# Performance work log

Hardware: AMD Instinct MI355X
Metric: run time of the kernel (lower is better)

The kernel has to match this reference:

```python
import jax, jax.numpy as jnp
import numpy as np

DIM = 1024
E = 8
HID = 4 * DIM  # DomainExpert FFN hidden size


def setup_inputs() -> dict:
    key = jax.random.key(0)
    ks = jax.random.split(key, 7)
    x = jax.random.normal(ks[0], (1, 2048, DIM), dtype=jnp.float32)
    Wr = jax.random.normal(ks[1], (DIM, E), dtype=jnp.float32) * (DIM ** -0.5)
    br = jnp.zeros((E,), dtype=jnp.float32)
    W1 = jax.random.normal(ks[2], (E, DIM, HID), dtype=jnp.float32) * (DIM ** -0.5)
    b1 = jnp.zeros((E, 1, HID), dtype=jnp.float32)
    W2 = jax.random.normal(ks[3], (E, HID, DIM), dtype=jnp.float32) * (HID ** -0.5)
    b2 = jnp.zeros((E, 1, DIM), dtype=jnp.float32)
    return {"x": x, "Wr": Wr, "br": br, "W1": W1, "b1": b1, "W2": W2, "b2": b2}


def reference(x, Wr, br, W1, b1, W2, b2):
    B, T, D = x.shape
    flat = x.reshape(B * T, D)                       # [N, D]
    logits = flat @ Wr + br                          # [N, E]
    z_loss = jnp.mean(jax.nn.logsumexp(logits, axis=-1) ** 2)
    probs = jax.nn.softmax(logits, axis=-1)          # eval path (no Gumbel)
    top_p, top_i = jax.lax.top_k(probs, 2)           # [N, 2]
    top_p = top_p / (top_p.sum(-1, keepdims=True) + 1e-12)
    N = flat.shape[0]
    nE = Wr.shape[1]
    # combine weights: w[t, e] = renormalized top-2 prob if e selected, else 0
    w = jnp.zeros((N, nE), dtype=flat.dtype).at[
        jnp.arange(N)[:, None], top_i].add(top_p)   # [N, E]
    # dense (jit-friendly) expert compute; combine masks out unselected experts
    h = jax.nn.gelu(jnp.einsum('td,edh->teh', flat, W1) + b1.transpose(1, 0, 2))  # [N, E, HID]
    y = jnp.einsum('teh,ehd->ted', h, W2) + b2.transpose(1, 0, 2)                 # [N, E, D]
    out = jnp.einsum('ted,te->td', y, w).reshape(B, T, D)
    importance = probs.mean(axis=0)                                               # [E]
    fi = jax.nn.one_hot(top_i, nE, dtype=flat.dtype).sum(axis=1).mean(axis=0)     # [E]
    aux_loss = jnp.asarray(nE, flat.dtype) * (importance * fi).sum()
    return out, z_loss, aux_loss
```

## Files before the change

kernel.cpp:

```cpp
#include <hip/hip_runtime.h>
#include <math.h>

#define N_TOK 2048
#define DIM   1024
#define NEXP  8
#define HID   4096
#define TOTPAIR (2 * N_TOK)

#define BM 128
#define BN 128
#define BK 32
#define KSPLIT2 4

typedef __bf16 bf16x8 __attribute__((ext_vector_type(8)));
typedef __bf16 bf16x4 __attribute__((ext_vector_type(4)));
typedef float  f32x4  __attribute__((ext_vector_type(4)));

__device__ __forceinline__ float gelu_tanh(float v) {
    float a = 0.7978845608028654f * (v + 0.044715f * v * v * v);
    a = fminf(fmaxf(a, -15.f), 15.f);
    float t = __expf(-2.f * a);
    return 0.5f * v * (1.f + (1.f - t) / (1.f + t));
}

__device__ __forceinline__ void stage16(const __bf16* g, __bf16* lds_base, int lane) {
#if defined(__has_builtin) && __has_builtin(__builtin_amdgcn_global_load_lds)
    __builtin_amdgcn_global_load_lds((const __attribute__((address_space(1))) void*)g,
                                     (__attribute__((address_space(3))) void*)lds_base,
                                     16, 0, 0);
#else
    *(bf16x8*)((char*)lds_base + (size_t)lane * 16) = *(const bf16x8*)g;
#endif
}

__device__ __forceinline__ int expert_prefix(const int* cnt, int e) {
    int s = 0;
    for (int i = 0; i < NEXP; i++) s += (i < e) ? cnt[i] : 0;
    return s;
}

__device__ __forceinline__ void router_body(
    int t, int lane,
    const float* __restrict__ x, const float* __restrict__ Wr, const float* __restrict__ br,
    float* __restrict__ probs, float* __restrict__ lsq,
    int* __restrict__ cnt, int* __restrict__ tok, float* __restrict__ wl) {
    const float* xr = x + (size_t)t * DIM;
    float acc[NEXP];
#pragma unroll
    for (int e = 0; e < NEXP; e++) acc[e] = 0.f;
    for (int d = lane; d < DIM; d += 64) {
        float xv = xr[d];
        const float* wr = Wr + (size_t)d * NEXP;
#pragma unroll
        for (int e = 0; e < NEXP; e++) acc[e] = fmaf(xv, wr[e], acc[e]);
    }
#pragma unroll
    for (int off = 32; off >= 1; off >>= 1) {
#pragma unroll
        for (int e = 0; e < NEXP; e++) acc[e] += __shfl_xor(acc[e], off, 64);
    }
    if (lane == 0) {
        float lg[NEXP], mx = -1e30f;
#pragma unroll
        for (int e = 0; e < NEXP; e++) { lg[e] = acc[e] + br[e]; mx = fmaxf(mx, lg[e]); }
        float se = 0.f, p[NEXP];
#pragma unroll
        for (int e = 0; e < NEXP; e++) { p[e] = expf(lg[e] - mx); se += p[e]; }
        float inv = 1.f / se;
        float lse = mx + logf(se);
        lsq[t] = lse * lse;
#pragma unroll
        for (int e = 0; e < NEXP; e++) probs[t * NEXP + e] = p[e] * inv;
        int i0 = 0;
#pragma unroll
        for (int e = 1; e < NEXP; e++) if (p[e] > p[i0]) i0 = e;
        int i1 = (i0 == 0) ? 1 : 0;
#pragma unroll
        for (int e = 0; e < NEXP; e++) if (e != i0 && p[e] > p[i1]) i1 = e;
        float p0 = p[i0] * inv, p1 = p[i1] * inv;
        float rn = 1.f / (p0 + p1 + 1e-12f);
        int pos0 = atomicAdd(&cnt[i0], 1);
        tok[i0 * N_TOK + pos0] = t;
        wl[i0 * N_TOK + pos0] = p0 * rn;
        int pos1 = atomicAdd(&cnt[i1], 1);
        tok[i1 * N_TOK + pos1] = t;
        wl[i1 * N_TOK + pos1] = p1 * rn;
    }
}

__global__ void router_kernel(const float* __restrict__ x, const float* __restrict__ Wr,
                              const float* __restrict__ br,
                              float* __restrict__ probs, float* __restrict__ lsq,
                              int* __restrict__ cnt, int* __restrict__ tok,
                              float* __restrict__ wl) {
    router_body(blockIdx.x, threadIdx.x, x, Wr, br, probs, lsq, cnt, tok, wl);
}

__global__ __launch_bounds__(256) void prep_kernel(
    const float* __restrict__ x, const float* __restrict__ Wr, const float* __restrict__ br,
    float* __restrict__ probs, float* __restrict__ lsq,
    int* __restrict__ cnt, int* __restrict__ tok, float* __restrict__ wl,
    __bf16* __restrict__ xb) {
    const int b = blockIdx.x;
    const int tid = threadIdx.x;
    if (b < 512) {
        int t = b * 4 + (tid >> 6);
        router_body(t, tid & 63, x, Wr, br, probs, lsq, cnt, tok, wl);
        return;
    }
    int idx = (b - 512) * 256 + tid;
    float4 v = ((const float4*)x)[idx];
    bf16x4 o;
    o.x = (__bf16)v.x; o.y = (__bf16)v.y; o.z = (__bf16)v.z; o.w = (__bf16)v.w;
    ((bf16x4*)xb)[idx] = o;
}

__global__ __launch_bounds__(256, 4) void gemm1_kernel(
    const __bf16* __restrict__ xb, const float* __restrict__ W1,
    const float* __restrict__ b1,
    const int* __restrict__ cnt,
    const int* __restrict__ tok, __bf16* __restrict__ h) {
    const int e = blockIdx.z;
    const int ce = cnt[e];
    const int mstart = blockIdx.y * BM;
    if (mstart >= ce) return;
    const int n0 = blockIdx.x * BN;
    const int offe = expert_prefix(cnt, e);

    __shared__ __bf16 smem[BM * 128];
    __shared__ int toksh[BM];
    __bf16* As = smem;
    __bf16* Bs = smem + 4096;

    const int tid = threadIdx.x;
    if (tid < BM) {
        int idx = mstart + tid;
        toksh[tid] = (idx < ce) ? tok[e * N_TOK + idx] : 0;
    }
    __syncthreads();

    const int lane = tid & 63;
    const int wid  = tid >> 6;
    const int row0 = (wid >> 1) * 64;
    const int col0 = (wid & 1) * 64;
    const int quad = lane >> 4;
    const int lcol = lane & 15;

    const int sub = lane >> 2;
    const int gk  = (((lane & 3) ^ (sub & 3)) << 3);
    const int ra0 = wid * 32 + sub;
    const int ra1 = ra0 + 16;
    const __bf16* pA0 = xb + (size_t)toksh[ra0] * DIM + gk;
    const __bf16* pA1 = xb + (size_t)toksh[ra1] * DIM + gk;
    __bf16* lA0 = &As[(wid * 2 + 0) * 512];
    __bf16* lA1 = &As[(wid * 2 + 1) * 512];

    const int khalf = (wid >> 1) * 16;
    const int nl    = (wid & 1) * 64 + lane;
    const float* __restrict__ W1e = W1 + (size_t)e * DIM * HID;
    const float* wsrc = W1e + (size_t)khalf * HID + n0 + nl;

    const int aswz = (quad ^ (lcol & 3)) << 3;
    const __bf16* aF = &As[(row0 + lcol) * BK + aswz];

    f32x4 acc[4][4];
#pragma unroll
    for (int i = 0; i < 4; i++)
#pragma unroll
        for (int j = 0; j < 4; j++) acc[i][j] = (f32x4){0.f, 0.f, 0.f, 0.f};

    for (int k0 = 0; k0 < DIM; k0 += BK) {
        float v[16];
        const float* ws = wsrc + (size_t)k0 * HID;
#pragma unroll
        for (int j = 0; j < 16; j++) v[j] = ws[(size_t)j * HID];
        stage16(pA0 + k0, lA0, lane);
        stage16(pA1 + k0, lA1, lane);
#pragma unroll
        for (int q = 0; q < 4; q++) {
            bf16x4 pk;
            pk.x = (__bf16)v[q * 4 + 0]; pk.y = (__bf16)v[q * 4 + 1];
            pk.z = (__bf16)v[q * 4 + 2]; pk.w = (__bf16)v[q * 4 + 3];
            int c = (wid >> 1) * 2 + (q >> 1);
            int slot = c ^ (nl & 3);
            *(bf16x4*)&Bs[slot * 1024 + nl * 8 + (q & 1) * 4] = pk;
        }
        __syncthreads();
        bf16x8 af[4], bfr[4];
#pragma unroll
        for (int i = 0; i < 4; i++) af[i]  = *(const bf16x8*)(aF + i * 16 * BK);
#pragma unroll
        for (int j = 0; j < 4; j++)
            bfr[j] = *(const bf16x8*)&Bs[((quad ^ (lcol & 3)) * 1024) + (col0 + j * 16 + lcol) * 8];
#pragma unroll
        for (int i = 0; i < 4; i++)
#pragma unroll
            for (int j = 0; j < 4; j++)
                acc[i][j] = __builtin_amdgcn_mfma_f32_16x16x32_bf16(af[i], bfr[j], acc[i][j], 0, 0, 0);
        __syncthreads();
    }

    const float* __restrict__ b1e = b1 + (size_t)e * HID;
    float bj[4];
#pragma unroll
    for (int j = 0; j < 4; j++) bj[j] = b1e[n0 + col0 + j * 16 + lcol];
#pragma unroll
    for (int i = 0; i < 4; i++)
#pragma unroll
        for (int reg = 0; reg < 4; reg++) {
            int row = row0 + i * 16 + quad * 4 + reg;
#pragma unroll
            for (int j = 0; j < 4; j++) {
                int col = col0 + j * 16 + lcol;
                int slot = (col >> 3) ^ (row & 15);
                smem[row * 128 + slot * 8 + (col & 7)] =
                    (__bf16)gelu_tanh(acc[i][j][reg] + bj[j]);
            }
        }
    __syncthreads();
    {
        int row = tid >> 1, half = tid & 1;
        int pos = mstart + row;
        if (pos < ce) {
            __bf16* hp = h + (size_t)(offe + pos) * HID + n0 + half * 64;
#pragma unroll
            for (int j = 0; j < 8; j++) {
                int chunk = half * 8 + j;
                int slot = chunk ^ (row & 15);
                *(bf16x8*)(hp + j * 8) = *(const bf16x8*)&smem[row * 128 + slot * 8];
            }
        }
    }
}

__global__ __launch_bounds__(256, 4) void gemm2_kernel(
    const __bf16* __restrict__ h, const float* __restrict__ W2,
    const float* __restrict__ b2,
    const int* __restrict__ cnt,
    const int* __restrict__ tok, const float* __restrict__ wl,
    float* __restrict__ out) {
    const int e = blockIdx.z >> 2;
    const int split = blockIdx.z & 3;
    const int ce = cnt[e];
    const int mstart = blockIdx.y * BM;
    if (mstart >= ce) return;
    const int n0 = blockIdx.x * BN;
    const int ks = split * (HID / KSPLIT2);
    const int offe = expert_prefix(cnt, e);

    __shared__ __bf16 As[BM * BK];
    __shared__ __bf16 Bs[4 * 128 * 8];
    __shared__ int   toksh[BM];
    __shared__ float wsh[BM];

    const int tid = threadIdx.x;
    if (tid < BM) {
        int idx = mstart + tid;
        toksh[tid] = (idx < ce) ? tok[e * N_TOK + idx] : 0;
        wsh[tid]   = (idx < ce) ? wl[e * N_TOK + idx] : 0.f;
    }
    __syncthreads();

    const int lane = tid & 63;
    const int wid  = tid >> 6;
    const int row0 = (wid >> 1) * 64;
    const int col0 = (wid & 1) * 64;
    const int quad = lane >> 4;
    const int lcol = lane & 15;

    const int sub = lane >> 2;
    const int gk  = (((lane & 3) ^ (sub & 3)) << 3);
    const int ra0 = wid * 32 + sub;
    const int ra1 = ra0 + 16;
    int hr0 = offe + mstart + ra0; if (hr0 >= TOTPAIR) hr0 = TOTPAIR - 1;
    int hr1 = offe + mstart + ra1; if (hr1 >= TOTPAIR) hr1 = TOTPAIR - 1;
    const __bf16* pA0 = h + (size_t)hr0 * HID + ks + gk;
    const __bf16* pA1 = h + (size_t)hr1 * HID + ks + gk;
    __bf16* lA0 = &As[(wid * 2 + 0) * 512];
    __bf16* lA1 = &As[(wid * 2 + 1) * 512];

    const int khalf = (wid >> 1) * 16;
    const int nl    = (wid & 1) * 64 + lane;
    const float* __restrict__ W2e = W2 + (size_t)e * HID * DIM;
    const float* wsrc = W2e + (size_t)(ks + khalf) * DIM + n0 + nl;

    const int aswz = (quad ^ (lcol & 3)) << 3;
    const __bf16* aF = &As[(row0 + lcol) * BK + aswz];

    f32x4 acc[4][4];
#pragma unroll
    for (int i = 0; i < 4; i++)
#pragma unroll
        for (int j = 0; j < 4; j++) acc[i][j] = (f32x4){0.f, 0.f, 0.f, 0.f};

    for (int k0 = 0; k0 < HID / KSPLIT2; k0 += BK) {
        float v[16];
        const float* ws = wsrc + (size_t)k0 * DIM;
#pragma unroll
        for (int j = 0; j < 16; j++) v[j] = ws[(size_t)j * DIM];
        stage16(pA0 + k0, lA0, lane);
        stage16(pA1 + k0, lA1, lane);
#pragma unroll
        for (int q = 0; q < 4; q++) {
            bf16x4 pk;
            pk.x = (__bf16)v[q * 4 + 0]; pk.y = (__bf16)v[q * 4 + 1];
            pk.z = (__bf16)v[q * 4 + 2]; pk.w = (__bf16)v[q * 4 + 3];
            int c = (wid >> 1) * 2 + (q >> 1);
            int slot = c ^ (nl & 3);
            *(bf16x4*)&Bs[slot * 1024 + nl * 8 + (q & 1) * 4] = pk;
        }
        __syncthreads();
        bf16x8 af[4], bfr[4];
#pragma unroll
        for (int i = 0; i < 4; i++) af[i]  = *(const bf16x8*)(aF + i * 16 * BK);
#pragma unroll
        for (int j = 0; j < 4; j++)
            bfr[j] = *(const bf16x8*)&Bs[((quad ^ (lcol & 3)) * 1024) + (col0 + j * 16 + lcol) * 8];
#pragma unroll
        for (int i = 0; i < 4; i++)
#pragma unroll
            for (int j = 0; j < 4; j++)
                acc[i][j] = __builtin_amdgcn_mfma_f32_16x16x32_bf16(af[i], bfr[j], acc[i][j], 0, 0, 0);
        __syncthreads();
    }

    const float* __restrict__ b2e = b2 + (size_t)e * DIM;
    const bool addBias = (split == 0);
#pragma unroll
    for (int i = 0; i < 4; i++) {
#pragma unroll
        for (int reg = 0; reg < 4; reg++) {
            int lrow = row0 + i * 16 + quad * 4 + reg;
            int pos = mstart + lrow;
            if (pos >= ce) continue;
            int tokm = toksh[lrow];
            float w = wsh[lrow];
#pragma unroll
            for (int j = 0; j < 4; j++) {
                int gcol = n0 + col0 + j * 16 + lcol;
                float vv = acc[i][j][reg] + (addBias ? b2e[gcol] : 0.f);
                atomicAdd(&out[(size_t)tokm * DIM + gcol], w * vv);
            }
        }
    }
}

__global__ __launch_bounds__(256, 2) void ffn_fallback_kernel(
    const float* __restrict__ x,
    const float* __restrict__ W1, const float* __restrict__ b1,
    const float* __restrict__ W2, const float* __restrict__ b2,
    const int* __restrict__ cnt, const int* __restrict__ tok,
    const float* __restrict__ wl, float* __restrict__ out) {
    const int e = blockIdx.y;
    const int ce = cnt[e];
    const int start = blockIdx.x * 16;
    if (start >= ce) return;
    __shared__ float hs[16][128];
    __shared__ int toks[16];
    __shared__ float wgt[16];
    const int tid = threadIdx.x;
    if (tid < 16) {
        int idx = start + tid;
        if (idx < ce) { toks[tid] = tok[e * N_TOK + idx]; wgt[tid] = wl[e * N_TOK + idx]; }
        else          { toks[tid] = -1;                   wgt[tid] = 0.f; }
    }
    __syncthreads();
    const float* __restrict__ W1e = W1 + (size_t)e * DIM * HID;
    const float* __restrict__ W2e = W2 + (size_t)e * HID * DIM;
    const int am  = tid >> 4;
    const int aj0 = (tid & 15) * 8;
    const int at  = toks[am];
    const float* __restrict__ xrow = x + (size_t)(at < 0 ? 0 : at) * DIM;
    const int n0 = tid * 4;
    float acc[16][4];
#pragma unroll
    for (int m = 0; m < 16; m++)
#pragma unroll
        for (int i = 0; i < 4; i++) acc[m][i] = 0.f;
    for (int c = 0; c < HID; c += 128) {
        float ha[8];
#pragma unroll
        for (int r = 0; r < 8; r++) ha[r] = 0.f;
        const float* wp = W1e + c + aj0;
        for (int d = 0; d < DIM; d += 4) {
            float4 xv = *(const float4*)(xrow + d);
#pragma unroll
            for (int k = 0; k < 4; k++) {
                const float* wr = wp + (size_t)(d + k) * HID;
                float4 wa = *(const float4*)(wr);
                float4 wb = *(const float4*)(wr + 4);
                float xk = (k == 0) ? xv.x : (k == 1) ? xv.y : (k == 2) ? xv.z : xv.w;
                ha[0] = fmaf(xk, wa.x, ha[0]); ha[1] = fmaf(xk, wa.y, ha[1]);
                ha[2] = fmaf(xk, wa.z, ha[2]); ha[3] = fmaf(xk, wa.w, ha[3]);
                ha[4] = fmaf(xk, wb.x, ha[4]); ha[5] = fmaf(xk, wb.y, ha[5]);
                ha[6] = fmaf(xk, wb.z, ha[6]); ha[7] = fmaf(xk, wb.w, ha[7]);
            }
        }
        __syncthreads();
#pragma unroll
        for (int r = 0; r < 8; r++) {
            float v = ha[r] + b1[e * HID + c + aj0 + r];
            hs[am][aj0 + r] = gelu_tanh(v);
        }
        __syncthreads();
        for (int jj = 0; jj < 128; jj++) {
            float4 wv = *(const float4*)(W2e + (size_t)(c + jj) * DIM + n0);
#pragma unroll
            for (int m = 0; m < 16; m++) {
                float hv = hs[m][jj];
                acc[m][0] = fmaf(hv, wv.x, acc[m][0]); acc[m][1] = fmaf(hv, wv.y, acc[m][1]);
                acc[m][2] = fmaf(hv, wv.z, acc[m][2]); acc[m][3] = fmaf(hv, wv.w, acc[m][3]);
            }
        }
    }
    const float* bp = b2 + e * DIM + n0;
    float b0 = bp[0], b1v = bp[1], b2v = bp[2], b3 = bp[3];
#pragma unroll 1
    for (int m = 0; m < 16; m++) {
        int t = toks[m];
        if (t < 0) continue;
        float w = wgt[m];
        float* op = out + (size_t)t * DIM + n0;
        atomicAdd(op + 0, w * (acc[m][0] + b0));
        atomicAdd(op + 1, w * (acc[m][1] + b1v));
        atomicAdd(op + 2, w * (acc[m][2] + b2v));
        atomicAdd(op + 3, w * (acc[m][3] + b3));
    }
}

__global__ void finalize_kernel(const float* __restrict__ probs, const float* __restrict__ lsq,
                                const int* __restrict__ cnt, float* __restrict__ scal) {
    __shared__ float part[256][9];
    const int tid = threadIdx.x;
    float z = 0.f;
    float im[NEXP];
#pragma unroll
    for (int e = 0; e < NEXP; e++) im[e] = 0.f;
    for (int t = tid; t < N_TOK; t += 256) {
        z += lsq[t];
#pragma unroll
        for (int e = 0; e < NEXP; e++) im[e] += probs[t * NEXP + e];
    }
    part[tid][0] = z;
#pragma unroll
    for (int e = 0; e < NEXP; e++) part[tid][1 + e] = im[e];
    __syncthreads();
    if (tid == 0) {
        float zs = 0.f, ims[NEXP];
        for (int e = 0; e < NEXP; e++) ims[e] = 0.f;
        for (int i = 0; i < 256; i++) {
            zs += part[i][0];
            for (int e = 0; e < NEXP; e++) ims[e] += part[i][1 + e];
        }
        float nInv = 1.0f / (float)N_TOK;
        float aux = 0.f;
        for (int e = 0; e < NEXP; e++) aux += (ims[e] * nInv) * ((float)cnt[e] * nInv);
        scal[0] = zs * nInv;
        scal[1] = (float)NEXP * aux;
    }
}

extern "C" void kernel_launch(void* const* d_in, const int* in_sizes, int n_in,
                              void* d_out, int out_size, void* d_ws, size_t ws_size,
                              hipStream_t stream) {
    const float* x  = (const float*)d_in[0];
    const float* Wr = (const float*)d_in[1];
    const float* br = (const float*)d_in[2];
    const float* W1 = (const float*)d_in[3];
    const float* b1 = (const float*)d_in[4];
    const float* W2 = (const float*)d_in[5];
    const float* b2 = (const float*)d_in[6];
    float* out = (float*)d_out;

    char* base = (char*)d_ws;
    int*   cnt   = (int*)(base);
    int*   tokp  = (int*)(base + 64);
    float* wlp   = (float*)(base + 64 + 65536);
    float* probs = (float*)(base + 64 + 2 * 65536);
    float* lsq   = (float*)(base + 64 + 3 * 65536);
    const size_t SMALL_END = 64 + 3 * 65536 + 8192;
    __bf16* xb   = (__bf16*)(base + SMALL_END);
    __bf16* hbuf = (__bf16*)(base + SMALL_END + 4194304ull);
    const size_t REQ = SMALL_END + 4194304ull + 33554432ull;

    hipMemsetAsync(base, 0, 64, stream);
    hipMemsetAsync(d_out, 0, (size_t)out_size * sizeof(float), stream);

    if (ws_size >= REQ) {
        prep_kernel<<<512 + 2048, 256, 0, stream>>>(
            x, Wr, br, probs, lsq, cnt, tokp, wlp, xb);
        gemm1_kernel<<<dim3(HID / BN, N_TOK / BM, NEXP), 256, 0, stream>>>(
            xb, W1, b1, cnt, tokp, hbuf);
        gemm2_kernel<<<dim3(DIM / BN, N_TOK / BM, NEXP * KSPLIT2), 256, 0, stream>>>(
            hbuf, W2, b2, cnt, tokp, wlp, out);
    } else {
        router_kernel<<<N_TOK, 64, 0, stream>>>(x, Wr, br, probs, lsq, cnt, tokp, wlp);
        ffn_fallback_kernel<<<dim3(128, NEXP), 256, 0, stream>>>(
            x, W1, b1, W2, b2, cnt, tokp, wlp, out);
    }

    finalize_kernel<<<1, 256, 0, stream>>>(probs, lsq, cnt, out + (size_t)N_TOK * DIM);
}
```

Baseline: 545.2 us.

## Double-buffer LDS tiles in both expert GEMMs to overlap loads with MFMA

Both grouped GEMM kernels now keep two LDS buffers for the A (activations) and B (fp32 weights converted to bf16) tiles. The next k-slice is fetched into registers/LDS while MFMAs run on the current one, and one barrier per iteration is removed. This is meant to hide global load latency. The cost is more LDS per block (gemm2 grows to 32KB) and more live registers, so launch bounds drop occupancy from 4 to 3 blocks per SM.

```diff
diff --git a/kernel.cpp b/kernel.cpp
--- a/kernel.cpp
+++ b/kernel.cpp
@@ -115,7 +115,7 @@
     ((bf16x4*)xb)[idx] = o;
 }
 
-__global__ __launch_bounds__(256, 4) void gemm1_kernel(
+__global__ __launch_bounds__(256, 3) void gemm1_kernel(
     const __bf16* __restrict__ xb, const float* __restrict__ W1,
     const float* __restrict__ b1,
     const int* __restrict__ cnt,
@@ -129,8 +129,6 @@
 
     __shared__ __bf16 smem[BM * 128];
     __shared__ int toksh[BM];
-    __bf16* As = smem;
-    __bf16* Bs = smem + 4096;
 
     const int tid = threadIdx.x;
     if (tid < BM) {
@@ -152,8 +150,6 @@
     const int ra1 = ra0 + 16;
     const __bf16* pA0 = xb + (size_t)toksh[ra0] * DIM + gk;
     const __bf16* pA1 = xb + (size_t)toksh[ra1] * DIM + gk;
-    __bf16* lA0 = &As[(wid * 2 + 0) * 512];
-    __bf16* lA1 = &As[(wid * 2 + 1) * 512];
 
     const int khalf = (wid >> 1) * 16;
     const int nl    = (wid & 1) * 64 + lane;
@@ -161,7 +157,6 @@
     const float* wsrc = W1e + (size_t)khalf * HID + n0 + nl;
 
     const int aswz = (quad ^ (lcol & 3)) << 3;
-    const __bf16* aF = &As[(row0 + lcol) * BK + aswz];
 
     f32x4 acc[4][4];
 #pragma unroll
@@ -169,34 +164,62 @@
 #pragma unroll
         for (int j = 0; j < 4; j++) acc[i][j] = (f32x4){0.f, 0.f, 0.f, 0.f};
 
-    for (int k0 = 0; k0 < DIM; k0 += BK) {
+    stage16(pA0, &smem[(wid * 2 + 0) * 512], lane);
+    stage16(pA1, &smem[(wid * 2 + 1) * 512], lane);
+    {
         float v[16];
-        const float* ws = wsrc + (size_t)k0 * HID;
-#pragma unroll
-        for (int j = 0; j < 16; j++) v[j] = ws[(size_t)j * HID];
-        stage16(pA0 + k0, lA0, lane);
-        stage16(pA1 + k0, lA1, lane);
+#pragma unroll
+        for (int j = 0; j < 16; j++) v[j] = wsrc[(size_t)j * HID];
 #pragma unroll
         for (int q = 0; q < 4; q++) {
             bf16x4 pk;
             pk.x = (__bf16)v[q * 4 + 0]; pk.y = (__bf16)v[q * 4 + 1];
             pk.z = (__bf16)v[q * 4 + 2]; pk.w = (__bf16)v[q * 4 + 3];
-            int c = (wid >> 1) * 2 + (q >> 1);
-            int slot = c ^ (nl & 3);
-            *(bf16x4*)&Bs[slot * 1024 + nl * 8 + (q & 1) * 4] = pk;
-        }
-        __syncthreads();
+            int cch  = (wid >> 1) * 2 + (q >> 1);
+            int slot = cch ^ (nl & 3);
+            *(bf16x4*)&smem[8192 + slot * 1024 + nl * 8 + (q & 1) * 4] = pk;
+        }
+    }
+    __syncthreads();
+
+    const int NK = DIM / BK;
+    for (int k = 0; k < NK; ++k) {
+        const int c = k & 1;
+        const bool pf = (k + 1 < NK);
+        float v[16];
+        if (pf) {
+            const int k1 = (k + 1) * BK;
+            stage16(pA0 + k1, &smem[(c ^ 1) * 4096 + (wid * 2 + 0) * 512], lane);
+            stage16(pA1 + k1, &smem[(c ^ 1) * 4096 + (wid * 2 + 1) * 512], lane);
+            const float* ws = wsrc + (size_t)(k + 1) * BK * HID;
+#pragma unroll
+            for (int j = 0; j < 16; j++) v[j] = ws[(size_t)j * HID];
+        }
+        const __bf16* Acur = &smem[c * 4096];
+        const __bf16* Bcur = &smem[8192 + c * 4096];
+        const __bf16* aF = &Acur[(row0 + lcol) * BK + aswz];
         bf16x8 af[4], bfr[4];
 #pragma unroll
         for (int i = 0; i < 4; i++) af[i]  = *(const bf16x8*)(aF + i * 16 * BK);
 #pragma unroll
         for (int j = 0; j < 4; j++)
-            bfr[j] = *(const bf16x8*)&Bs[((quad ^ (lcol & 3)) * 1024) + (col0 + j * 16 + lcol) * 8];
+            bfr[j] = *(const bf16x8*)&Bcur[((quad ^ (lcol & 3)) * 1024) + (col0 + j * 16 + lcol) * 8];
 #pragma unroll
         for (int i = 0; i < 4; i++)
 #pragma unroll
             for (int j = 0; j < 4; j++)
                 acc[i][j] = __builtin_amdgcn_mfma_f32_16x16x32_bf16(af[i], bfr[j], acc[i][j], 0, 0, 0);
+        if (pf) {
+#pragma unroll
+            for (int q = 0; q < 4; q++) {
+                bf16x4 pk;
+                pk.x = (__bf16)v[q * 4 + 0]; pk.y = (__bf16)v[q * 4 + 1];
+                pk.z = (__bf16)v[q * 4 + 2]; pk.w = (__bf16)v[q * 4 + 3];
+                int cch  = (wid >> 1) * 2 + (q >> 1);
+                int slot = cch ^ (nl & 3);
+                *(bf16x4*)&smem[8192 + (c ^ 1) * 4096 + slot * 1024 + nl * 8 + (q & 1) * 4] = pk;
+            }
+        }
         __syncthreads();
     }
 
@@ -233,7 +256,7 @@
     }
 }
 
-__global__ __launch_bounds__(256, 4) void gemm2_kernel(
+__global__ __launch_bounds__(256, 3) void gemm2_kernel(
     const __bf16* __restrict__ h, const float* __restrict__ W2,
     const float* __restrict__ b2,
     const int* __restrict__ cnt,
@@ -248,8 +271,7 @@
     const int ks = split * (HID / KSPLIT2);
     const int offe = expert_prefix(cnt, e);
 
-    __shared__ __bf16 As[BM * BK];
-    __shared__ __bf16 Bs[4 * 128 * 8];
+    __shared__ __bf16 smem[4 * 4096];
     __shared__ int   toksh[BM];
     __shared__ float wsh[BM];
 
@@ -276,8 +298,6 @@
     int hr1 = offe + mstart + ra1; if (hr1 >= TOTPAIR) hr1 = TOTPAIR - 1;
     const __bf16* pA0 = h + (size_t)hr0 * HID + ks + gk;
     const __bf16* pA1 = h + (size_t)hr1 * HID + ks + gk;
-    __bf16* lA0 = &As[(wid * 2 + 0) * 512];
-    __bf16* lA1 = &As[(wid * 2 + 1) * 512];
 
     const int khalf = (wid >> 1) * 16;
     const int nl    = (wid & 1) * 64 + lane;
@@ -285,7 +305,6 @@
     const float* wsrc = W2e + (size_t)(ks + khalf) * DIM + n0 + nl;
 
     const int aswz = (quad ^ (lcol & 3)) << 3;
-    const __bf16* aF = &As[(row0 + lcol) * BK + aswz];
 
     f32x4 acc[4][4];
 #pragma unroll
@@ -293,34 +312,62 @@
 #pragma unroll
         for (int j = 0; j < 4; j++) acc[i][j] = (f32x4){0.f, 0.f, 0.f, 0.f};
 
-    for (int k0 = 0; k0 < HID / KSPLIT2; k0 += BK) {
+    stage16(pA0, &smem[(wid * 2 + 0) * 512], lane);
+    stage16(pA1, &smem[(wid * 2 + 1) * 512], lane);
+    {
         float v[16];
-        const float* ws = wsrc + (size_t)k0 * DIM;
-#pragma unroll
-        for (int j = 0; j < 16; j++) v[j] = ws[(size_t)j * DIM];
-        stage16(pA0 + k0, lA0, lane);
-        stage16(pA1 + k0, lA1, lane);
+#pragma unroll
+        for (int j = 0; j < 16; j++) v[j] = wsrc[(size_t)j * DIM];
 #pragma unroll
         for (int q = 0; q < 4; q++) {
             bf16x4 pk;
             pk.x = (__bf16)v[q * 4 + 0]; pk.y = (__bf16)v[q * 4 + 1];
             pk.z = (__bf16)v[q * 4 + 2]; pk.w = (__bf16)v[q * 4 + 3];
-            int c = (wid >> 1) * 2 + (q >> 1);
-            int slot = c ^ (nl & 3);
-            *(bf16x4*)&Bs[slot * 1024 + nl * 8 + (q & 1) * 4] = pk;
-        }
-        __syncthreads();
+            int cch  = (wid >> 1) * 2 + (q >> 1);
+            int slot = cch ^ (nl & 3);
+            *(bf16x4*)&smem[8192 + slot * 1024 + nl * 8 + (q & 1) * 4] = pk;
+        }
+    }
+    __syncthreads();
+
+    const int NK = (HID / KSPLIT2) / BK;
+    for (int k = 0; k < NK; ++k) {
+        const int c = k & 1;
+        const bool pf = (k + 1 < NK);
+        float v[16];
+        if (pf) {
+            const int k1 = (k + 1) * BK;
+            stage16(pA0 + k1, &smem[(c ^ 1) * 4096 + (wid * 2 + 0) * 512], lane);
+            stage16(pA1 + k1, &smem[(c ^ 1) * 4096 + (wid * 2 + 1) * 512], lane);
+            const float* ws = wsrc + (size_t)(k + 1) * BK * DIM;
+#pragma unroll
+            for (int j = 0; j < 16; j++) v[j] = ws[(size_t)j * DIM];
+        }
+        const __bf16* Acur = &smem[c * 4096];
+        const __bf16* Bcur = &smem[8192 + c * 4096];
+        const __bf16* aF = &Acur[(row0 + lcol) * BK + aswz];
         bf16x8 af[4], bfr[4];
 #pragma unroll
         for (int i = 0; i < 4; i++) af[i]  = *(const bf16x8*)(aF + i * 16 * BK);
 #pragma unroll
         for (int j = 0; j < 4; j++)
-            bfr[j] = *(const bf16x8*)&Bs[((quad ^ (lcol & 3)) * 1024) + (col0 + j * 16 + lcol) * 8];
+            bfr[j] = *(const bf16x8*)&Bcur[((quad ^ (lcol & 3)) * 1024) + (col0 + j * 16 + lcol) * 8];
 #pragma unroll
         for (int i = 0; i < 4; i++)
 #pragma unroll
             for (int j = 0; j < 4; j++)
                 acc[i][j] = __builtin_amdgcn_mfma_f32_16x16x32_bf16(af[i], bfr[j], acc[i][j], 0, 0, 0);
+        if (pf) {
+#pragma unroll
+            for (int q = 0; q < 4; q++) {
+                bf16x4 pk;
+                pk.x = (__bf16)v[q * 4 + 0]; pk.y = (__bf16)v[q * 4 + 1];
+                pk.z = (__bf16)v[q * 4 + 2]; pk.w = (__bf16)v[q * 4 + 3];
+                int cch  = (wid >> 1) * 2 + (q >> 1);
+                int slot = cch ^ (nl & 3);
+                *(bf16x4*)&smem[8192 + (c ^ 1) * 4096 + slot * 1024 + nl * 8 + (q & 1) * 4] = pk;
+            }
+        }
         __syncthreads();
     }
 
```

Result: slower. 560.0 us (+2.7%).

## Enlarge expert GEMM tiles to 256x256 with 512-thread blocks

Applied to the files above, without the earlier changes.

Both expert GEMMs move from 128x128 tiles with 4 waves to 256x256 tiles with 8 waves. Each wave now holds a 128x64 accumulator, which raises data reuse per staged weight and activation tile and halves the global reads of the fp32 weights per output. The GEMM1 epilogue is staged through shared memory in four 64-row chunks to fit the LDS buffer. The finalize kernel swaps its serial 256-entry sum for a tree reduction. The cost is higher register pressure, lower occupancy, and fewer blocks, which leaves more tail waste on partially filled per-expert tiles.

```diff
diff --git a/kernel.cpp b/kernel.cpp
--- a/kernel.cpp
+++ b/kernel.cpp
@@ -7,8 +7,6 @@
 #define HID   4096
 #define TOTPAIR (2 * N_TOK)
 
-#define BM 128
-#define BN 128
 #define BK 32
 #define KSPLIT2 4
 
@@ -115,25 +113,25 @@
     ((bf16x4*)xb)[idx] = o;
 }
 
-__global__ __launch_bounds__(256, 4) void gemm1_kernel(
+__global__ __launch_bounds__(512, 2) void gemm1_kernel(
     const __bf16* __restrict__ xb, const float* __restrict__ W1,
     const float* __restrict__ b1,
     const int* __restrict__ cnt,
     const int* __restrict__ tok, __bf16* __restrict__ h) {
     const int e = blockIdx.z;
     const int ce = cnt[e];
-    const int mstart = blockIdx.y * BM;
+    const int mstart = blockIdx.y * 256;
     if (mstart >= ce) return;
-    const int n0 = blockIdx.x * BN;
+    const int n0 = blockIdx.x * 256;
     const int offe = expert_prefix(cnt, e);
 
-    __shared__ __bf16 smem[BM * 128];
-    __shared__ int toksh[BM];
+    __shared__ __bf16 smem[16384];
+    __shared__ int toksh[256];
     __bf16* As = smem;
-    __bf16* Bs = smem + 4096;
+    __bf16* Bs = smem + 8192;
 
     const int tid = threadIdx.x;
-    if (tid < BM) {
+    if (tid < 256) {
         int idx = mstart + tid;
         toksh[tid] = (idx < ce) ? tok[e * N_TOK + idx] : 0;
     }
@@ -141,8 +139,8 @@
 
     const int lane = tid & 63;
     const int wid  = tid >> 6;
-    const int row0 = (wid >> 1) * 64;
-    const int col0 = (wid & 1) * 64;
+    const int row0 = (wid >> 2) * 128;
+    const int col0 = (wid & 3) * 64;
     const int quad = lane >> 4;
     const int lcol = lane & 15;
 
@@ -155,17 +153,17 @@
     __bf16* lA0 = &As[(wid * 2 + 0) * 512];
     __bf16* lA1 = &As[(wid * 2 + 1) * 512];
 
-    const int khalf = (wid >> 1) * 16;
-    const int nl    = (wid & 1) * 64 + lane;
+    const int khalf = (wid >> 2) * 16;
+    const int nl    = (wid & 3) * 64 + lane;
     const float* __restrict__ W1e = W1 + (size_t)e * DIM * HID;
     const float* wsrc = W1e + (size_t)khalf * HID + n0 + nl;
 
     const int aswz = (quad ^ (lcol & 3)) << 3;
     const __bf16* aF = &As[(row0 + lcol) * BK + aswz];
 
-    f32x4 acc[4][4];
-#pragma unroll
-    for (int i = 0; i < 4; i++)
+    f32x4 acc[8][4];
+#pragma unroll
+    for (int i = 0; i < 8; i++)
 #pragma unroll
         for (int j = 0; j < 4; j++) acc[i][j] = (f32x4){0.f, 0.f, 0.f, 0.f};
 
@@ -181,19 +179,19 @@
             bf16x4 pk;
             pk.x = (__bf16)v[q * 4 + 0]; pk.y = (__bf16)v[q * 4 + 1];
             pk.z = (__bf16)v[q * 4 + 2]; pk.w = (__bf16)v[q * 4 + 3];
-            int c = (wid >> 1) * 2 + (q >> 1);
-            int slot = c ^ (nl & 3);
-            *(bf16x4*)&Bs[slot * 1024 + nl * 8 + (q & 1) * 4] = pk;
-        }
-        __syncthreads();
-        bf16x8 af[4], bfr[4];
-#pragma unroll
-        for (int i = 0; i < 4; i++) af[i]  = *(const bf16x8*)(aF + i * 16 * BK);
+            int cch  = (wid >> 2) * 2 + (q >> 1);
+            int slot = cch ^ (nl & 3);
+            *(bf16x4*)&Bs[slot * 2048 + nl * 8 + (q & 1) * 4] = pk;
+        }
+        __syncthreads();
+        bf16x8 af[8], bfr[4];
+#pragma unroll
+        for (int i = 0; i < 8; i++) af[i] = *(const bf16x8*)(aF + i * 16 * BK);
 #pragma unroll
         for (int j = 0; j < 4; j++)
-            bfr[j] = *(const bf16x8*)&Bs[((quad ^ (lcol & 3)) * 1024) + (col0 + j * 16 + lcol) * 8];
-#pragma unroll
-        for (int i = 0; i < 4; i++)
+            bfr[j] = *(const bf16x8*)&Bs[((quad ^ (lcol & 3)) * 2048) + (col0 + j * 16 + lcol) * 8];
+#pragma unroll
+        for (int i = 0; i < 8; i++)
 #pragma unroll
             for (int j = 0; j < 4; j++)
                 acc[i][j] = __builtin_amdgcn_mfma_f32_16x16x32_bf16(af[i], bfr[j], acc[i][j], 0, 0, 0);
@@ -204,36 +202,45 @@
     float bj[4];
 #pragma unroll
     for (int j = 0; j < 4; j++) bj[j] = b1e[n0 + col0 + j * 16 + lcol];
-#pragma unroll
-    for (int i = 0; i < 4; i++)
-#pragma unroll
-        for (int reg = 0; reg < 4; reg++) {
-            int row = row0 + i * 16 + quad * 4 + reg;
-#pragma unroll
-            for (int j = 0; j < 4; j++) {
-                int col = col0 + j * 16 + lcol;
-                int slot = (col >> 3) ^ (row & 15);
-                smem[row * 128 + slot * 8 + (col & 7)] =
-                    (__bf16)gelu_tanh(acc[i][j][reg] + bj[j]);
+    const int mg = wid >> 2;
+#pragma unroll 1
+    for (int cch = 0; cch < 4; ++cch) {
+        if ((cch >> 1) == mg) {
+            const int ibase = (cch & 1) * 4;
+#pragma unroll
+            for (int ii = 0; ii < 4; ii++) {
+#pragma unroll
+                for (int reg = 0; reg < 4; reg++) {
+                    int lrow = ii * 16 + quad * 4 + reg;
+#pragma unroll
+                    for (int j = 0; j < 4; j++) {
+                        int col = col0 + j * 16 + lcol;
+                        int slot = (col >> 3) ^ (lrow & 15);
+                        smem[lrow * 256 + slot * 8 + (col & 7)] =
+                            (__bf16)gelu_tanh(acc[ibase + ii][j][reg] + bj[j]);
+                    }
+                }
             }
         }
-    __syncthreads();
-    {
-        int row = tid >> 1, half = tid & 1;
-        int pos = mstart + row;
-        if (pos < ce) {
-            __bf16* hp = h + (size_t)(offe + pos) * HID + n0 + half * 64;
-#pragma unroll
-            for (int j = 0; j < 8; j++) {
-                int chunk = half * 8 + j;
-                int slot = chunk ^ (row & 15);
-                *(bf16x8*)(hp + j * 8) = *(const bf16x8*)&smem[row * 128 + slot * 8];
+        __syncthreads();
+        {
+            int r = tid >> 3, cb = (tid & 7) * 32;
+            int pos = mstart + cch * 64 + r;
+            if (pos < ce) {
+                __bf16* hp = h + (size_t)(offe + pos) * HID + n0 + cb;
+#pragma unroll
+                for (int j2 = 0; j2 < 4; j2++) {
+                    int colc = cb + j2 * 8;
+                    int slot = (colc >> 3) ^ (r & 15);
+                    *(bf16x8*)(hp + j2 * 8) = *(const bf16x8*)&smem[r * 256 + slot * 8];
+                }
             }
         }
-    }
-}
-
-__global__ __launch_bounds__(256, 4) void gemm2_kernel(
+        __syncthreads();
+    }
+}
+
+__global__ __launch_bounds__(512, 2) void gemm2_kernel(
     const __bf16* __restrict__ h, const float* __restrict__ W2,
     const float* __restrict__ b2,
     const int* __restrict__ cnt,
@@ -242,19 +249,20 @@
     const int e = blockIdx.z >> 2;
     const int split = blockIdx.z & 3;
     const int ce = cnt[e];
-    const int mstart = blockIdx.y * BM;
+    const int mstart = blockIdx.y * 256;
     if (mstart >= ce) return;
-    const int n0 = blockIdx.x * BN;
+    const int n0 = blockIdx.x * 256;
     const int ks = split * (HID / KSPLIT2);
     const int offe = expert_prefix(cnt, e);
 
-    __shared__ __bf16 As[BM * BK];
-    __shared__ __bf16 Bs[4 * 128 * 8];
-    __shared__ int   toksh[BM];
-    __shared__ float wsh[BM];
+    __shared__ __bf16 smem[16384];
+    __shared__ int   toksh[256];
+    __shared__ float wsh[256];
+    __bf16* As = smem;
+    __bf16* Bs = smem + 8192;
 
     const int tid = threadIdx.x;
-    if (tid < BM) {
+    if (tid < 256) {
         int idx = mstart + tid;
         toksh[tid] = (idx < ce) ? tok[e * N_TOK + idx] : 0;
         wsh[tid]   = (idx < ce) ? wl[e * N_TOK + idx] : 0.f;
@@ -263,8 +271,8 @@
 
     const int lane = tid & 63;
     const int wid  = tid >> 6;
-    const int row0 = (wid >> 1) * 64;
-    const int col0 = (wid & 1) * 64;
+    const int row0 = (wid >> 2) * 128;
+    const int col0 = (wid & 3) * 64;
     const int quad = lane >> 4;
     const int lcol = lane & 15;
 
@@ -279,17 +287,17 @@
     __bf16* lA0 = &As[(wid * 2 + 0) * 512];
     __bf16* lA1 = &As[(wid * 2 + 1) * 512];
 
-    const int khalf = (wid >> 1) * 16;
-    const int nl    = (wid & 1) * 64 + lane;
+    const int khalf = (wid >> 2) * 16;
+    const int nl    = (wid & 3) * 64 + lane;
     const float* __restrict__ W2e = W2 + (size_t)e * HID * DIM;
     const float* wsrc = W2e + (size_t)(ks + khalf) * DIM + n0 + nl;
 
     const int aswz = (quad ^ (lcol & 3)) << 3;
     const __bf16* aF = &As[(row0 + lcol) * BK + aswz];
 
-    f32x4 acc[4][4];
-#pragma unroll
-    for (int i = 0; i < 4; i++)
+    f32x4 acc[8][4];
+#pragma unroll
+    for (int i = 0; i < 8; i++)
 #pragma unroll
         for (int j = 0; j < 4; j++) acc[i][j] = (f32x4){0.f, 0.f, 0.f, 0.f};
 
@@ -305,19 +313,19 @@
             bf16x4 pk;
             pk.x = (__bf16)v[q * 4 + 0]; pk.y = (__bf16)v[q * 4 + 1];
             pk.z = (__bf16)v[q * 4 + 2]; pk.w = (__bf16)v[q * 4 + 3];
-            int c = (wid >> 1) * 2 + (q >> 1);
-            int slot = c ^ (nl & 3);
-            *(bf16x4*)&Bs[slot * 1024 + nl * 8 + (q & 1) * 4] = pk;
-        }
-        __syncthreads();
-        bf16x8 af[4], bfr[4];
-#pragma unroll
-        for (int i = 0; i < 4; i++) af[i]  = *(const bf16x8*)(aF + i * 16 * BK);
+            int cch  = (wid >> 2) * 2 + (q >> 1);
+            int slot = cch ^ (nl & 3);
+            *(bf16x4*)&Bs[slot * 2048 + nl * 8 + (q & 1) * 4] = pk;
+        }
+        __syncthreads();
+        bf16x8 af[8], bfr[4];
+#pragma unroll
+        for (int i = 0; i < 8; i++) af[i] = *(const bf16x8*)(aF + i * 16 * BK);
 #pragma unroll
         for (int j = 0; j < 4; j++)
-            bfr[j] = *(const bf16x8*)&Bs[((quad ^ (lcol & 3)) * 1024) + (col0 + j * 16 + lcol) * 8];
-#pragma unroll
-        for (int i = 0; i < 4; i++)
+            bfr[j] = *(const bf16x8*)&Bs[((quad ^ (lcol & 3)) * 2048) + (col0 + j * 16 + lcol) * 8];
+#pragma unroll
+        for (int i = 0; i < 8; i++)
 #pragma unroll
             for (int j = 0; j < 4; j++)
                 acc[i][j] = __builtin_amdgcn_mfma_f32_16x16x32_bf16(af[i], bfr[j], acc[i][j], 0, 0, 0);
@@ -327,7 +335,7 @@
     const float* __restrict__ b2e = b2 + (size_t)e * DIM;
     const bool addBias = (split == 0);
 #pragma unroll
-    for (int i = 0; i < 4; i++) {
+    for (int i = 0; i < 8; i++) {
 #pragma unroll
         for (int reg = 0; reg < 4; reg++) {
             int lrow = row0 + i * 16 + quad * 4 + reg;
@@ -445,17 +453,18 @@
 #pragma unroll
     for (int e = 0; e < NEXP; e++) part[tid][1 + e] = im[e];
     __syncthreads();
+    for (int off = 128; off >= 1; off >>= 1) {
+        if (tid < off) {
+#pragma unroll
+            for (int s = 0; s < 9; s++) part[tid][s] += part[tid + off][s];
+        }
+        __syncthreads();
+    }
     if (tid == 0) {
-        float zs = 0.f, ims[NEXP];
-        for (int e = 0; e < NEXP; e++) ims[e] = 0.f;
-        for (int i = 0; i < 256; i++) {
-            zs += part[i][0];
-            for (int e = 0; e < NEXP; e++) ims[e] += part[i][1 + e];
-        }
         float nInv = 1.0f / (float)N_TOK;
         float aux = 0.f;
-        for (int e = 0; e < NEXP; e++) aux += (ims[e] * nInv) * ((float)cnt[e] * nInv);
-        scal[0] = zs * nInv;
+        for (int e = 0; e < NEXP; e++) aux += (part[0][1 + e] * nInv) * ((float)cnt[e] * nInv);
+        scal[0] = part[0][0] * nInv;
         scal[1] = (float)NEXP * aux;
     }
 }
@@ -489,9 +498,9 @@
     if (ws_size >= REQ) {
         prep_kernel<<<512 + 2048, 256, 0, stream>>>(
             x, Wr, br, probs, lsq, cnt, tokp, wlp, xb);
-        gemm1_kernel<<<dim3(HID / BN, N_TOK / BM, NEXP), 256, 0, stream>>>(
+        gemm1_kernel<<<dim3(HID / 256, N_TOK / 256, NEXP), 512, 0, stream>>>(
             xb, W1, b1, cnt, tokp, hbuf);
-        gemm2_kernel<<<dim3(DIM / BN, N_TOK / BM, NEXP * KSPLIT2), 256, 0, stream>>>(
+        gemm2_kernel<<<dim3(DIM / 256, N_TOK / 256, NEXP * KSPLIT2), 512, 0, stream>>>(
             hbuf, W2, b2, cnt, tokp, wlp, out);
     } else {
         router_kernel<<<N_TOK, 64, 0, stream>>>(x, Wr, br, probs, lsq, cnt, tokp, wlp);
```

Result: slower. 1.530 ms (+180.5%).

## Double-buffer LDS and register-prefetch weights in both expert GEMMs

Applied to the files above, without the earlier changes.

Both grouped GEMM main loops become a software pipeline. A-tiles are staged into a ping-pong LDS buffer one step ahead, fp32 weights are prefetched into alternating register arrays two steps ahead, and each step ends with a partial vmcnt wait plus a single barrier instead of two syncthreads. The aim is to hide global-load latency behind the MFMA work. In exchange, LDS per block doubles and extra registers are held, so launch bounds drop from 4 to 3 blocks per SM. The finalize kernel also replaces its serial 256-way reduction with a tree reduction.

```diff
diff --git a/kernel.cpp b/kernel.cpp
--- a/kernel.cpp
+++ b/kernel.cpp
@@ -115,7 +115,68 @@
     ((bf16x4*)xb)[idx] = o;
 }
 
-__global__ __launch_bounds__(256, 4) void gemm1_kernel(
+#define GEMM_PIPE_PROLOGUE(LDB)                                                     \
+    stage16(pA0, &As[(wid * 2 + 0) * 512], lane);                                   \
+    stage16(pA1, &As[(wid * 2 + 1) * 512], lane);                                   \
+    {                                                                               \
+        float v0_[16];                                                              \
+        _Pragma("unroll")                                                           \
+        for (int j_ = 0; j_ < 16; j_++) v0_[j_] = wsrc[(size_t)j_ * (LDB)];         \
+        _Pragma("unroll")                                                           \
+        for (int q_ = 0; q_ < 4; q_++) {                                            \
+            bf16x4 pk_;                                                             \
+            pk_.x = (__bf16)v0_[q_ * 4 + 0]; pk_.y = (__bf16)v0_[q_ * 4 + 1];       \
+            pk_.z = (__bf16)v0_[q_ * 4 + 2]; pk_.w = (__bf16)v0_[q_ * 4 + 3];       \
+            int cch_  = (wid >> 1) * 2 + (q_ >> 1);                                 \
+            int slot_ = cch_ ^ (nl & 3);                                            \
+            *(bf16x4*)&Bs[slot_ * 1024 + nl * 8 + (q_ & 1) * 4] = pk_;              \
+        }                                                                           \
+    }                                                                               \
+    _Pragma("unroll")                                                               \
+    for (int j_ = 0; j_ < 16; j_++) vA[j_] = wsrc[(size_t)(BK + j_) * (LDB)];       \
+    asm volatile("s_waitcnt vmcnt(16) lgkmcnt(0)" ::: "memory");                    \
+    __builtin_amdgcn_s_barrier();                                                   \
+    __builtin_amdgcn_sched_barrier(0);
+
+#define GEMM_PIPE_ITER(K, VIN, VOUT, LDB)                                           \
+    {                                                                               \
+        const int c_  = (K) & 1;                                                    \
+        const int kn1 = ((K) + 1) & 31;                                             \
+        const int kn2 = ((K) + 2) & 31;                                             \
+        stage16(pA0 + kn1 * BK, &As[(c_ ^ 1) * 4096 + (wid * 2 + 0) * 512], lane);  \
+        stage16(pA1 + kn1 * BK, &As[(c_ ^ 1) * 4096 + (wid * 2 + 1) * 512], lane);  \
+        const float* wsn_ = wsrc + (size_t)(kn2 * BK) * (LDB);                      \
+        _Pragma("unroll")                                                           \
+        for (int j_ = 0; j_ < 16; j_++) VOUT[j_] = wsn_[(size_t)j_ * (LDB)];        \
+        const __bf16* Acur_ = &As[c_ * 4096];                                       \
+        const __bf16* Bcur_ = &Bs[c_ * 4096];                                       \
+        const __bf16* aFc_  = &Acur_[(row0 + lcol) * BK + aswz];                    \
+        bf16x8 af_[4], bfr_[4];                                                     \
+        _Pragma("unroll")                                                           \
+        for (int i_ = 0; i_ < 4; i_++) af_[i_] = *(const bf16x8*)(aFc_ + i_ * 16 * BK); \
+        _Pragma("unroll")                                                           \
+        for (int j_ = 0; j_ < 4; j_++)                                              \
+            bfr_[j_] = *(const bf16x8*)&Bcur_[((quad ^ (lcol & 3)) * 1024) + (col0 + j_ * 16 + lcol) * 8]; \
+        _Pragma("unroll")                                                           \
+        for (int i_ = 0; i_ < 4; i_++)                                              \
+            _Pragma("unroll")                                                       \
+            for (int j_ = 0; j_ < 4; j_++)                                          \
+                acc[i_][j_] = __builtin_amdgcn_mfma_f32_16x16x32_bf16(af_[i_], bfr_[j_], acc[i_][j_], 0, 0, 0); \
+        _Pragma("unroll")                                                           \
+        for (int q_ = 0; q_ < 4; q_++) {                                            \
+            bf16x4 pk_;                                                             \
+            pk_.x = (__bf16)VIN[q_ * 4 + 0]; pk_.y = (__bf16)VIN[q_ * 4 + 1];       \
+            pk_.z = (__bf16)VIN[q_ * 4 + 2]; pk_.w = (__bf16)VIN[q_ * 4 + 3];       \
+            int cch_  = (wid >> 1) * 2 + (q_ >> 1);                                 \
+            int slot_ = cch_ ^ (nl & 3);                                            \
+            *(bf16x4*)&Bs[(c_ ^ 1) * 4096 + slot_ * 1024 + nl * 8 + (q_ & 1) * 4] = pk_; \
+        }                                                                           \
+        asm volatile("s_waitcnt vmcnt(16) lgkmcnt(0)" ::: "memory");                \
+        __builtin_amdgcn_s_barrier();                                               \
+        __builtin_amdgcn_sched_barrier(0);                                          \
+    }
+
+__global__ __launch_bounds__(256, 3) void gemm1_kernel(
     const __bf16* __restrict__ xb, const float* __restrict__ W1,
     const float* __restrict__ b1,
     const int* __restrict__ cnt,
@@ -130,7 +191,7 @@
     __shared__ __bf16 smem[BM * 128];
     __shared__ int toksh[BM];
     __bf16* As = smem;
-    __bf16* Bs = smem + 4096;
+    __bf16* Bs = smem + 8192;
 
     const int tid = threadIdx.x;
     if (tid < BM) {
@@ -152,8 +213,6 @@
     const int ra1 = ra0 + 16;
     const __bf16* pA0 = xb + (size_t)toksh[ra0] * DIM + gk;
     const __bf16* pA1 = xb + (size_t)toksh[ra1] * DIM + gk;
-    __bf16* lA0 = &As[(wid * 2 + 0) * 512];
-    __bf16* lA1 = &As[(wid * 2 + 1) * 512];
 
     const int khalf = (wid >> 1) * 16;
     const int nl    = (wid & 1) * 64 + lane;
@@ -161,7 +220,6 @@
     const float* wsrc = W1e + (size_t)khalf * HID + n0 + nl;
 
     const int aswz = (quad ^ (lcol & 3)) << 3;
-    const __bf16* aF = &As[(row0 + lcol) * BK + aswz];
 
     f32x4 acc[4][4];
 #pragma unroll
@@ -169,36 +227,14 @@
 #pragma unroll
         for (int j = 0; j < 4; j++) acc[i][j] = (f32x4){0.f, 0.f, 0.f, 0.f};
 
-    for (int k0 = 0; k0 < DIM; k0 += BK) {
-        float v[16];
-        const float* ws = wsrc + (size_t)k0 * HID;
-#pragma unroll
-        for (int j = 0; j < 16; j++) v[j] = ws[(size_t)j * HID];
-        stage16(pA0 + k0, lA0, lane);
-        stage16(pA1 + k0, lA1, lane);
-#pragma unroll
-        for (int q = 0; q < 4; q++) {
-            bf16x4 pk;
-            pk.x = (__bf16)v[q * 4 + 0]; pk.y = (__bf16)v[q * 4 + 1];
-            pk.z = (__bf16)v[q * 4 + 2]; pk.w = (__bf16)v[q * 4 + 3];
-            int c = (wid >> 1) * 2 + (q >> 1);
-            int slot = c ^ (nl & 3);
-            *(bf16x4*)&Bs[slot * 1024 + nl * 8 + (q & 1) * 4] = pk;
-        }
-        __syncthreads();
-        bf16x8 af[4], bfr[4];
-#pragma unroll
-        for (int i = 0; i < 4; i++) af[i]  = *(const bf16x8*)(aF + i * 16 * BK);
-#pragma unroll
-        for (int j = 0; j < 4; j++)
-            bfr[j] = *(const bf16x8*)&Bs[((quad ^ (lcol & 3)) * 1024) + (col0 + j * 16 + lcol) * 8];
-#pragma unroll
-        for (int i = 0; i < 4; i++)
-#pragma unroll
-            for (int j = 0; j < 4; j++)
-                acc[i][j] = __builtin_amdgcn_mfma_f32_16x16x32_bf16(af[i], bfr[j], acc[i][j], 0, 0, 0);
-        __syncthreads();
-    }
+    float vA[16], vB[16];
+    GEMM_PIPE_PROLOGUE(HID)
+#pragma unroll 1
+    for (int k = 0; k < 32; k += 2) {
+        GEMM_PIPE_ITER(k,     vA, vB, HID)
+        GEMM_PIPE_ITER(k + 1, vB, vA, HID)
+    }
+    __syncthreads();
 
     const float* __restrict__ b1e = b1 + (size_t)e * HID;
     float bj[4];
@@ -233,7 +269,7 @@
     }
 }
 
-__global__ __launch_bounds__(256, 4) void gemm2_kernel(
+__global__ __launch_bounds__(256, 3) void gemm2_kernel(
     const __bf16* __restrict__ h, const float* __restrict__ W2,
     const float* __restrict__ b2,
     const int* __restrict__ cnt,
@@ -248,10 +284,11 @@
     const int ks = split * (HID / KSPLIT2);
     const int offe = expert_prefix(cnt, e);
 
-    __shared__ __bf16 As[BM * BK];
-    __shared__ __bf16 Bs[4 * 128 * 8];
+    __shared__ __bf16 smem[4 * 4096];
     __shared__ int   toksh[BM];
     __shared__ float wsh[BM];
+    __bf16* As = smem;
+    __bf16* Bs = smem + 8192;
 
     const int tid = threadIdx.x;
     if (tid < BM) {
@@ -276,8 +313,6 @@
     int hr1 = offe + mstart + ra1; if (hr1 >= TOTPAIR) hr1 = TOTPAIR - 1;
     const __bf16* pA0 = h + (size_t)hr0 * HID + ks + gk;
     const __bf16* pA1 = h + (size_t)hr1 * HID + ks + gk;
-    __bf16* lA0 = &As[(wid * 2 + 0) * 512];
-    __bf16* lA1 = &As[(wid * 2 + 1) * 512];
 
     const int khalf = (wid >> 1) * 16;
     const int nl    = (wid & 1) * 64 + lane;
@@ -285,7 +320,6 @@
     const float* wsrc = W2e + (size_t)(ks + khalf) * DIM + n0 + nl;
 
     const int aswz = (quad ^ (lcol & 3)) << 3;
-    const __bf16* aF = &As[(row0 + lcol) * BK + aswz];
 
     f32x4 acc[4][4];
 #pragma unroll
@@ -293,36 +327,14 @@
 #pragma unroll
         for (int j = 0; j < 4; j++) acc[i][j] = (f32x4){0.f, 0.f, 0.f, 0.f};
 
-    for (int k0 = 0; k0 < HID / KSPLIT2; k0 += BK) {
-        float v[16];
-        const float* ws = wsrc + (size_t)k0 * DIM;
-#pragma unroll
-        for (int j = 0; j < 16; j++) v[j] = ws[(size_t)j * DIM];
-        stage16(pA0 + k0, lA0, lane);
-        stage16(pA1 + k0, lA1, lane);
-#pragma unroll
-        for (int q = 0; q < 4; q++) {
-            bf16x4 pk;
-            pk.x = (__bf16)v[q * 4 + 0]; pk.y = (__bf16)v[q * 4 + 1];
-            pk.z = (__bf16)v[q * 4 + 2]; pk.w = (__bf16)v[q * 4 + 3];
-            int c = (wid >> 1) * 2 + (q >> 1);
-            int slot = c ^ (nl & 3);
-            *(bf16x4*)&Bs[slot * 1024 + nl * 8 + (q & 1) * 4] = pk;
-        }
-        __syncthreads();
-        bf16x8 af[4], bfr[4];
-#pragma unroll
-        for (int i = 0; i < 4; i++) af[i]  = *(const bf16x8*)(aF + i * 16 * BK);
-#pragma unroll
-        for (int j = 0; j < 4; j++)
-            bfr[j] = *(const bf16x8*)&Bs[((quad ^ (lcol & 3)) * 1024) + (col0 + j * 16 + lcol) * 8];
-#pragma unroll
-        for (int i = 0; i < 4; i++)
-#pragma unroll
-            for (int j = 0; j < 4; j++)
-                acc[i][j] = __builtin_amdgcn_mfma_f32_16x16x32_bf16(af[i], bfr[j], acc[i][j], 0, 0, 0);
-        __syncthreads();
-    }
+    float vA[16], vB[16];
+    GEMM_PIPE_PROLOGUE(DIM)
+#pragma unroll 1
+    for (int k = 0; k < 32; k += 2) {
+        GEMM_PIPE_ITER(k,     vA, vB, DIM)
+        GEMM_PIPE_ITER(k + 1, vB, vA, DIM)
+    }
+    __syncthreads();
 
     const float* __restrict__ b2e = b2 + (size_t)e * DIM;
     const bool addBias = (split == 0);
@@ -445,17 +457,18 @@
 #pragma unroll
     for (int e = 0; e < NEXP; e++) part[tid][1 + e] = im[e];
     __syncthreads();
+    for (int off = 128; off >= 1; off >>= 1) {
+        if (tid < off) {
+#pragma unroll
+            for (int s = 0; s < 9; s++) part[tid][s] += part[tid + off][s];
+        }
+        __syncthreads();
+    }
     if (tid == 0) {
-        float zs = 0.f, ims[NEXP];
-        for (int e = 0; e < NEXP; e++) ims[e] = 0.f;
-        for (int i = 0; i < 256; i++) {
-            zs += part[i][0];
-            for (int e = 0; e < NEXP; e++) ims[e] += part[i][1 + e];
-        }
         float nInv = 1.0f / (float)N_TOK;
         float aux = 0.f;
-        for (int e = 0; e < NEXP; e++) aux += (ims[e] * nInv) * ((float)cnt[e] * nInv);
-        scal[0] = zs * nInv;
+        for (int e = 0; e < NEXP; e++) aux += (part[0][1 + e] * nInv) * ((float)cnt[e] * nInv);
+        scal[0] = part[0][0] * nInv;
         scal[1] = (float)NEXP * aux;
     }
 }
```

Result: faster. 533.0 us (-2.2%).
